# Performance work log

Measured on AMD Instinct MI355X. Metric: run time of the kernel, lower is better.

The kernel has to match this reference:

```python
import jax, jax.numpy as jnp
import numpy as np

BLOCK_SIZE = 1024
OUTLIER_SIGMA = 3.0
OUT_FEATURES = 11008
IN_FEATURES = 4096
TOKENS = 64


def _quantize_mixed_np(W):
    """Faithful numpy port of quantize_mixed (BLOCK_SIZE divides numel exactly here)."""
    flat = W.astype(np.float32).reshape(-1)
    nb = flat.size // BLOCK_SIZE
    blocks = flat.reshape(nb, BLOCK_SIZE)
    mu = blocks.mean(axis=1, keepdims=True)
    sig = np.maximum(blocks.std(axis=1, ddof=1, keepdims=True), 1e-8)  # torch.std is unbiased
    outlier = np.abs(blocks - mu) > OUTLIER_SIGMA * sig
    abs_max = np.maximum(np.abs(np.where(outlier, 0.0, blocks)).max(axis=1), 1e-8)
    scales = (abs_max / 127.0).astype(np.float16)
    q = np.clip(np.round(blocks / abs_max[:, None] * 127.0), -127, 127).astype(np.int8)
    all_pos = np.arange(nb, dtype=np.int64)[:, None] * BLOCK_SIZE + np.arange(BLOCK_SIZE, dtype=np.int64)[None, :]
    int8_data = q[~outlier]                      # row-major == torch order
    fp16_data = blocks[outlier].astype(np.float16)
    int8_pos = all_pos[~outlier].astype(np.int32)
    fp16_pos = all_pos[outlier].astype(np.int32)
    block_idx = np.nonzero(~outlier)[0].astype(np.int32)  # block index per int8 value
    return int8_data, fp16_data, scales, int8_pos, fp16_pos, block_idx


def setup_inputs() -> dict:
    key = jax.random.key(0)
    k_x, k_b = jax.random.split(key)
    rng = np.random.default_rng(0)
    W = (rng.standard_normal((OUT_FEATURES, IN_FEATURES)) * 0.02).astype(np.float32)
    int8_data, fp16_data, scales, int8_pos, fp16_pos, block_idx = _quantize_mixed_np(W)
    x = jax.random.normal(k_x, (TOKENS, IN_FEATURES), dtype=jnp.float16)
    bias = jax.random.normal(k_b, (OUT_FEATURES,), dtype=jnp.float16) * jnp.float16(0.02)
    return {
        "x": x,
        "int8_data": jnp.asarray(int8_data),
        "fp16_data": jnp.asarray(fp16_data),
        "scales": jnp.asarray(scales),
        "bias": bias,
        "int8_pos": jnp.asarray(int8_pos),
        "fp16_pos": jnp.asarray(fp16_pos),
        "block_idx": jnp.asarray(block_idx),
    }


def reference(x, int8_data, fp16_data, scales, bias, int8_pos, fp16_pos, block_idx):
    out_features = bias.shape[0]
    in_features = x.shape[1]
    numel = out_features * in_features  # divisible by BLOCK_SIZE for these dims
    # dequantize_mixed: scatter fp16 outliers and dequantized int8 values into flat fp16 buffer
    flat = jnp.zeros((numel,), dtype=jnp.float16)
    flat = flat.at[fp16_pos].set(fp16_data)
    flat = flat.at[int8_pos].set(int8_data.astype(jnp.float16) * scales[block_idx])
    W = flat.reshape(out_features, in_features)
    # F.linear(x, W, bias) in fp16
    return jnp.dot(x.astype(jnp.float16), W.T) + bias
```

## Files before the change

kernel.cpp:

```cpp
#include <hip/hip_runtime.h>
#include <hip/hip_fp16.h>

#define TOK   64
#define INF   4096
#define OUTF  11008
#define NUMEL (OUTF * INF)
#define NSLC  (NUMEL / 64)
#define NQB   (NUMEL / 1024)
#define NBLK  (OUTF / 16)
#define KSPL  4

typedef __attribute__((ext_vector_type(8))) _Float16 half8;
typedef __attribute__((ext_vector_type(4))) _Float16 half4;
typedef __attribute__((ext_vector_type(4))) float floatx4;
typedef __attribute__((ext_vector_type(4), aligned(4))) int int4u;

__global__ __launch_bounds__(256) void precompute_kernel(
    const float* __restrict__ x, const int* __restrict__ fppos, int nf,
    _Float16* __restrict__ x16, int* __restrict__ cum64) {
  const int t = blockIdx.x * 256 + threadIdx.x;
  if (t < (TOK * INF) / 4) {
    const floatx4 f = *(const floatx4*)&x[t * 4];
    half4 h;
    h[0] = (_Float16)f[0]; h[1] = (_Float16)f[1];
    h[2] = (_Float16)f[2]; h[3] = (_Float16)f[3];
    *(half4*)&x16[t * 4] = h;
  }
  if (t <= NSLC) {
    const int target = t << 6;
    int lo = 0, hi = nf;
    while (lo < hi) {
      const int mid = (lo + hi) >> 1;
      if (fppos[mid] < target) lo = mid + 1; else hi = mid;
    }
    cum64[t] = lo;
  }
}

__global__ __launch_bounds__(256) void dequant_kernel(
    const int* __restrict__ i8, const float* __restrict__ fpdat,
    const int* __restrict__ fppos, const float* __restrict__ scales,
    const int* __restrict__ cum64, _Float16* __restrict__ W, int n8) {
  const int t   = blockIdx.x * 256 + threadIdx.x;
  const int p0  = t * 8;
  const int s64 = p0 >> 6;
  const int c0  = cum64[s64];
  const int c1  = cum64[s64 + 1];
  const float s = scales[p0 >> 10];

  int lt = 0, f = 0;
  float ov[8];
#pragma unroll
  for (int e = 0; e < 8; ++e) ov[e] = 0.f;

  const int w = c1 - c0;
  if (w > 0) {
    {
      const int d = fppos[c0] - p0;
      const float v = fpdat[c0];
      lt += (d < 0);
      if ((unsigned)d < 8u) {
        f |= 1 << d;
#pragma unroll
        for (int e = 0; e < 8; ++e) ov[e] = (d == e) ? v : ov[e];
      }
    }
    if (w > 1) {
      const int d = fppos[c0 + 1] - p0;
      const float v = fpdat[c0 + 1];
      lt += (d < 0);
      if ((unsigned)d < 8u) {
        f |= 1 << d;
#pragma unroll
        for (int e = 0; e < 8; ++e) ov[e] = (d == e) ? v : ov[e];
      }
    }
    for (int j = 2; j < w; ++j) {
      const int d = fppos[c0 + j] - p0;
      const float v = fpdat[c0 + j];
      lt += (d < 0);
      if ((unsigned)d < 8u) {
        f |= 1 << d;
#pragma unroll
        for (int e = 0; e < 8; ++e) ov[e] = (d == e) ? v : ov[e];
      }
    }
  }

  const int i0 = p0 - c0 - lt;
  half8 oh;
  if (i0 + 8 <= n8) {
    int l[8];
    *(int4u*)&l[0] = *(const int4u*)&i8[i0];
    *(int4u*)&l[4] = *(const int4u*)&i8[i0 + 4];
    if (f == 0) {
#pragma unroll
      for (int e = 0; e < 8; ++e) oh[e] = (_Float16)((float)l[e] * s);
    } else {
      int q = 0;
#pragma unroll
      for (int e = 0; e < 8; ++e) {
        const int flg = (f >> e) & 1;
        int lv = l[0];
#pragma unroll
        for (int qq = 1; qq < 8; ++qq) lv = (q == qq) ? l[qq] : lv;
        oh[e] = flg ? (_Float16)ov[e] : (_Float16)((float)lv * s);
        q += 1 - flg;
      }
    }
  } else {
    int c = 0;
    const int m = n8 - 1;
#pragma unroll
    for (int e = 0; e < 8; ++e) {
      const int flg = (f >> e) & 1;
      int idx = i0 + e - c;
      idx = idx < 0 ? 0 : (idx > m ? m : idx);
      oh[e] = flg ? (_Float16)ov[e] : (_Float16)((float)i8[idx] * s);
      c += flg;
    }
  }
  *(half8*)&W[p0] = oh;
}

__global__ __launch_bounds__(256) void gemm_kernel(
    const _Float16* __restrict__ x16, const _Float16* __restrict__ W,
    const float* __restrict__ bias, float* __restrict__ out) {
  __shared__ float red[4 * 64 * 16];

  const int tid  = threadIdx.x;
  const int wave = tid >> 6;
  const int lane = tid & 63;
  const int quad = lane >> 4;
  const int ln   = lane & 15;
  const int nt   = blockIdx.x >> 2;
  const int kq   = blockIdx.x & 3;
  const int n0   = nt * 16;

  const int kb = kq * 1024 + wave * 256 + quad * 8;
  const _Float16* wp = &W[(n0 + ln) * INF + kb];
  const _Float16* ap = &x16[ln * INF + kb];

  floatx4 acc0 = {0,0,0,0}, acc1 = {0,0,0,0}, acc2 = {0,0,0,0}, acc3 = {0,0,0,0};
#pragma unroll
  for (int st = 0; st < 8; ++st) {
    const int ko = st * 32;
    const half8 bh = *(const half8*)&wp[ko];
    const half8 a0 = *(const half8*)&ap[ko];
    const half8 a1 = *(const half8*)&ap[16 * INF + ko];
    const half8 a2 = *(const half8*)&ap[32 * INF + ko];
    const half8 a3 = *(const half8*)&ap[48 * INF + ko];
    acc0 = __builtin_amdgcn_mfma_f32_16x16x32_f16(a0, bh, acc0, 0, 0, 0);
    acc1 = __builtin_amdgcn_mfma_f32_16x16x32_f16(a1, bh, acc1, 0, 0, 0);
    acc2 = __builtin_amdgcn_mfma_f32_16x16x32_f16(a2, bh, acc2, 0, 0, 0);
    acc3 = __builtin_amdgcn_mfma_f32_16x16x32_f16(a3, bh, acc3, 0, 0, 0);
  }

  const int mb = quad * 4;
#pragma unroll
  for (int i = 0; i < 4; ++i) red[wave * 1024 + (mb + i)      * 16 + ln] = acc0[i];
#pragma unroll
  for (int i = 0; i < 4; ++i) red[wave * 1024 + (16 + mb + i) * 16 + ln] = acc1[i];
#pragma unroll
  for (int i = 0; i < 4; ++i) red[wave * 1024 + (32 + mb + i) * 16 + ln] = acc2[i];
#pragma unroll
  for (int i = 0; i < 4; ++i) red[wave * 1024 + (48 + mb + i) * 16 + ln] = acc3[i];
  __syncthreads();

#pragma unroll
  for (int c2 = 0; c2 < 4; ++c2) {
    const int cell = tid + c2 * 256;
    const int mm = cell >> 4, nn = cell & 15;
    float v = red[cell] + red[1024 + cell] + red[2048 + cell] + red[3072 + cell];
    if (kq == 0) v += bias[n0 + nn];
    atomicAdd(&out[mm * OUTF + n0 + nn], v);
  }
}

extern "C" void kernel_launch(void* const* d_in, const int* in_sizes, int n_in,
                              void* d_out, int out_size, void* d_ws,
                              size_t ws_size, hipStream_t stream) {
  const float* x      = (const float*)d_in[0];
  const int*   i8     = (const int*)d_in[1];
  const float* fpdat  = (const float*)d_in[2];
  const float* scales = (const float*)d_in[3];
  const float* bias   = (const float*)d_in[4];
  const int*   fppos  = (const int*)d_in[6];

  char* wsp = (char*)d_ws;
  _Float16* W     = (_Float16*)wsp;
  _Float16* x16   = (_Float16*)(wsp + (size_t)NUMEL * sizeof(_Float16));
  int*      cum64 = (int*)(wsp + (size_t)NUMEL * sizeof(_Float16)
                               + (size_t)TOK * INF * sizeof(_Float16));
  float*    out   = (float*)d_out;

  const int n8 = in_sizes[1];
  const int nf = in_sizes[2];

  hipMemsetAsync(out, 0, (size_t)out_size * sizeof(float), stream);
  precompute_kernel<<<(NSLC + 256) / 256 + 1, 256, 0, stream>>>(x, fppos, nf,
                                                                x16, cum64);
  dequant_kernel<<<NUMEL / (8 * 256), 256, 0, stream>>>(i8, fpdat, fppos,
                                                        scales, cum64, W, n8);
  gemm_kernel<<<NBLK * KSPL, 256, 0, stream>>>(x16, W, bias, out);
}
```

Before: 471.9 us.

## Fuse mixed int8/fp16 dequantization into GEMM B-operand loads

Removes the separate dequant kernel and the fp16 weight matrix staged in workspace. Each GEMM lane now rebuilds its 8-element weight slot on the fly from the int8 data, the outlier positions and the per-slice prefix counts, then feeds it straight into the MFMA. This cuts a full write and read-back of the ~90MB fp16 weight matrix and one launch. In exchange the GEMM inner loop carries irregular gathers and branching, and the unroll drops to 4, which can reduce MFMA overlap.

```diff
diff --git a/kernel.cpp b/kernel.cpp
--- a/kernel.cpp
+++ b/kernel.cpp
@@ -6,7 +6,6 @@
 #define OUTF  11008
 #define NUMEL (OUTF * INF)
 #define NSLC  (NUMEL / 64)
-#define NQB   (NUMEL / 1024)
 #define NBLK  (OUTF / 16)
 #define KSPL  4
 
@@ -37,16 +36,14 @@
   }
 }
 
-__global__ __launch_bounds__(256) void dequant_kernel(
+__device__ __forceinline__ half8 dq_slot(
+    const int p0, const float s,
     const int* __restrict__ i8, const float* __restrict__ fpdat,
-    const int* __restrict__ fppos, const float* __restrict__ scales,
-    const int* __restrict__ cum64, _Float16* __restrict__ W, int n8) {
-  const int t   = blockIdx.x * 256 + threadIdx.x;
-  const int p0  = t * 8;
+    const int* __restrict__ fppos, const int* __restrict__ cum64,
+    const int n8) {
   const int s64 = p0 >> 6;
   const int c0  = cum64[s64];
   const int c1  = cum64[s64 + 1];
-  const float s = scales[p0 >> 10];
 
   int lt = 0, f = 0;
   float ov[8];
@@ -120,12 +117,15 @@
       c += flg;
     }
   }
-  *(half8*)&W[p0] = oh;
-}
-
-__global__ __launch_bounds__(256) void gemm_kernel(
-    const _Float16* __restrict__ x16, const _Float16* __restrict__ W,
-    const float* __restrict__ bias, float* __restrict__ out) {
+  return oh;
+}
+
+__global__ __launch_bounds__(256) void gemm_fused(
+    const _Float16* __restrict__ x16,
+    const int* __restrict__ i8, const float* __restrict__ fpdat,
+    const int* __restrict__ fppos, const float* __restrict__ scales,
+    const int* __restrict__ cum64, const float* __restrict__ bias,
+    float* __restrict__ out, const int n8) {
   __shared__ float red[4 * 64 * 16];
 
   const int tid  = threadIdx.x;
@@ -136,16 +136,17 @@
   const int nt   = blockIdx.x >> 2;
   const int kq   = blockIdx.x & 3;
   const int n0   = nt * 16;
-
-  const int kb = kq * 1024 + wave * 256 + quad * 8;
-  const _Float16* wp = &W[(n0 + ln) * INF + kb];
+  const int row  = n0 + ln;
+  const int kb   = kq * 1024 + wave * 256 + quad * 8;
+  const int pb   = row * INF + kb;
+  const float s  = scales[row * 4 + kq];
   const _Float16* ap = &x16[ln * INF + kb];
 
   floatx4 acc0 = {0,0,0,0}, acc1 = {0,0,0,0}, acc2 = {0,0,0,0}, acc3 = {0,0,0,0};
-#pragma unroll
+#pragma unroll 4
   for (int st = 0; st < 8; ++st) {
     const int ko = st * 32;
-    const half8 bh = *(const half8*)&wp[ko];
+    const half8 bh = dq_slot(pb + ko, s, i8, fpdat, fppos, cum64, n8);
     const half8 a0 = *(const half8*)&ap[ko];
     const half8 a1 = *(const half8*)&ap[16 * INF + ko];
     const half8 a2 = *(const half8*)&ap[32 * INF + ko];
@@ -188,10 +189,8 @@
   const int*   fppos  = (const int*)d_in[6];
 
   char* wsp = (char*)d_ws;
-  _Float16* W     = (_Float16*)wsp;
-  _Float16* x16   = (_Float16*)(wsp + (size_t)NUMEL * sizeof(_Float16));
-  int*      cum64 = (int*)(wsp + (size_t)NUMEL * sizeof(_Float16)
-                               + (size_t)TOK * INF * sizeof(_Float16));
+  _Float16* x16   = (_Float16*)wsp;
+  int*      cum64 = (int*)(wsp + (size_t)TOK * INF * sizeof(_Float16));
   float*    out   = (float*)d_out;
 
   const int n8 = in_sizes[1];
@@ -200,7 +199,6 @@
   hipMemsetAsync(out, 0, (size_t)out_size * sizeof(float), stream);
   precompute_kernel<<<(NSLC + 256) / 256 + 1, 256, 0, stream>>>(x, fppos, nf,
                                                                 x16, cum64);
-  dequant_kernel<<<NUMEL / (8 * 256), 256, 0, stream>>>(i8, fpdat, fppos,
-                                                        scales, cum64, W, n8);
-  gemm_kernel<<<NBLK * KSPL, 256, 0, stream>>>(x16, W, bias, out);
-}
+  gemm_fused<<<NBLK * KSPL, 256, 0, stream>>>(x16, i8, fpdat, fppos, scales,
+                                              cum64, bias, out, n8);
+}
```

Result: no change. 467.0 us (-1.0%).
